# Kernel tuning notes

Hardware: AMD Instinct MI355X
Metric: run time of the kernel (lower is better)

## Reference

```python
import jax, jax.numpy as jnp
import numpy as np

N_HEADS = 16
D_EMBED = 1024
D_HEAD = D_EMBED // N_HEADS  # 64
B, S = 2, 2048


def setup_inputs() -> dict:
    key = jax.random.key(0)
    ks = jax.random.split(key, 6)
    k = jax.random.normal(ks[0], (B, S, D_EMBED), dtype=jnp.float32)
    q = jax.random.normal(ks[1], (B, S, D_EMBED), dtype=jnp.float32)
    v = jax.random.normal(ks[2], (B, S, D_EMBED), dtype=jnp.float32)
    # per-head projections, shared across heads (nn.Linear(d_head, d_head, bias=False))
    scale = 1.0 / np.sqrt(D_HEAD)
    Wk = jax.random.normal(ks[3], (D_HEAD, D_HEAD), dtype=jnp.float32) * scale
    Wq = jax.random.normal(ks[4], (D_HEAD, D_HEAD), dtype=jnp.float32) * scale
    Wv = jax.random.normal(ks[5], (D_HEAD, D_HEAD), dtype=jnp.float32) * scale
    return {"k": k, "q": q, "v": v, "Wk": Wk, "Wq": Wq, "Wv": Wv}


def reference(k, q, v, Wk, Wq, Wv):
    b, s, _ = k.shape
    # split heads: [b, s, h, dh]
    kh = k.reshape(b, s, N_HEADS, D_HEAD)
    qh = q.reshape(b, s, N_HEADS, D_HEAD)
    vh = v.reshape(b, s, N_HEADS, D_HEAD)
    # shared per-head linear projection (y = x @ W^T, torch Linear convention)
    kh = jnp.einsum('bshd,ed->bshe', kh, Wk)
    qh = jnp.einsum('bshd,ed->bshe', qh, Wq)
    vh = jnp.einsum('bshd,ed->bshe', vh, Wv)
    # attention scores [b, h, q, k]
    scores = jnp.einsum('bqhd,bkhd->bhqk', qh, kh) / np.sqrt(D_HEAD).astype(np.float32)
    attn = jax.nn.softmax(scores, axis=-1)
    out = jnp.einsum('bhqk,bkhd->bqhd', attn, vh)
    return out.reshape(b, s, D_EMBED)
```

## Files before the change

### kernel.cpp

```cpp
#include <hip/hip_runtime.h>
#include <hip/hip_bf16.h>

typedef unsigned short u16;
typedef __bf16 bf16x8 __attribute__((ext_vector_type(8)));
typedef float f32x4 __attribute__((ext_vector_type(4)));

#define S_LEN 2048
#define NH 16
#define NB 2
#define HEAD_ELEMS (NB * NH * S_LEN * 64)

#if __has_builtin(__builtin_amdgcn_exp2f)
#define EXP2(x) __builtin_amdgcn_exp2f(x)
#else
#define EXP2(x) exp2f(x)
#endif

#define QSCALE 0.180336880f
#define SHIFT2 30.0f

__device__ __forceinline__ bf16x8 pack8(float4 a, float4 b, float sc) {
    union { bf16x8 v; __hip_bfloat162 h[4]; } r;
    r.h[0] = __float22bfloat162_rn(make_float2(a.x * sc, a.y * sc));
    r.h[1] = __float22bfloat162_rn(make_float2(a.z * sc, a.w * sc));
    r.h[2] = __float22bfloat162_rn(make_float2(b.x * sc, b.y * sc));
    r.h[3] = __float22bfloat162_rn(make_float2(b.z * sc, b.w * sc));
    return r.v;
}

__global__ __launch_bounds__(256) void proj_kq(
    const float* __restrict__ kin, const float* __restrict__ qin,
    const float* __restrict__ Wk, const float* __restrict__ Wq,
    u16* __restrict__ Kh, u16* __restrict__ Qh)
{
    __shared__ __align__(16) u16 Yld[8 * 16 * 72];

    const int tid = threadIdx.x;
    const int wave = tid >> 6;
    const int lane = tid & 63;
    const int quad = lane >> 4;
    const int l15 = lane & 15;
    const int stile = blockIdx.x;
    const int p = blockIdx.y;
    const int hh = blockIdx.z;
    const long row0 = (long)stile * 16;
    const int b = (int)(row0 >> 11);
    const int s0 = (int)(row0 & 2047);

    const float* X = p ? qin : kin;
    const float* W = p ? Wq : Wk;
    const float sc = p ? QSCALE : 1.0f;

    const float* xr0 = X + (row0 + l15) * 1024 + (hh * 8 + wave * 2) * 64 + quad * 8;
    const float* xr1 = xr0 + 64;
    float4 xa[4], xb[4];
    xa[0] = *(const float4*)(xr0);      xa[1] = *(const float4*)(xr0 + 4);
    xa[2] = *(const float4*)(xr0 + 32); xa[3] = *(const float4*)(xr0 + 36);
    xb[0] = *(const float4*)(xr1);      xb[1] = *(const float4*)(xr1 + 4);
    xb[2] = *(const float4*)(xr1 + 32); xb[3] = *(const float4*)(xr1 + 36);

    bf16x8 wf[4][2];
    #pragma unroll
    for (int nt = 0; nt < 4; ++nt) {
        const float* wr = W + (nt * 16 + l15) * 64 + quad * 8;
        wf[nt][0] = pack8(*(const float4*)(wr),      *(const float4*)(wr + 4),  sc);
        wf[nt][1] = pack8(*(const float4*)(wr + 32), *(const float4*)(wr + 36), sc);
    }

    #pragma unroll
    for (int hp = 0; hp < 2; ++hp) {
        const int hl = wave * 2 + hp;
        bf16x8 a0 = pack8(hp ? xb[0] : xa[0], hp ? xb[1] : xa[1], 1.0f);
        bf16x8 a1 = pack8(hp ? xb[2] : xa[2], hp ? xb[3] : xa[3], 1.0f);
        #pragma unroll
        for (int nt = 0; nt < 4; ++nt) {
            f32x4 c = (f32x4){0.f, 0.f, 0.f, 0.f};
            c = __builtin_amdgcn_mfma_f32_16x16x32_bf16(a0, wf[nt][0], c, 0, 0, 0);
            c = __builtin_amdgcn_mfma_f32_16x16x32_bf16(a1, wf[nt][1], c, 0, 0, 0);
            union { __hip_bfloat162 h2; u16 u[2]; } x01, x23;
            x01.h2 = __float22bfloat162_rn(make_float2(c[0], c[1]));
            x23.h2 = __float22bfloat162_rn(make_float2(c[2], c[3]));
            int base = (hl * 16 + quad * 4) * 72 + nt * 16 + l15;
            Yld[base]       = x01.u[0];
            Yld[base + 72]  = x01.u[1];
            Yld[base + 144] = x23.u[0];
            Yld[base + 216] = x23.u[1];
        }
    }
    __syncthreads();

    u16* dst = p ? Qh : Kh;
    #pragma unroll
    for (int it = 0; it < 4; ++it) {
        int idx = tid + it * 256;
        int eg = idx & 7, s = (idx >> 3) & 15, hl = idx >> 7;
        int bh = b * NH + hh * 8 + hl;
        *(float4*)(dst + ((long)bh * S_LEN + s0 + s) * 64 + eg * 8) =
            *(const float4*)&Yld[(hl * 16 + s) * 72 + eg * 8];
    }
}

__global__ __launch_bounds__(256) void proj_v(
    const float* __restrict__ vin, const float* __restrict__ Wv, u16* __restrict__ Vt)
{
    __shared__ __align__(16) u16 Vtile[64 * 72];

    const int tid = threadIdx.x;
    const int wave = tid >> 6;
    const int lane = tid & 63;
    const int quad = lane >> 4;
    const int l15 = lane & 15;
    const long row0 = (long)blockIdx.x * 64;
    const int b = (int)(row0 >> 11);
    const int s0 = (int)(row0 & 2047);
    const int h = blockIdx.y;
    const int bh = b * NH + h;

    const float* xr = vin + (row0 + wave * 16 + l15) * 1024 + h * 64 + quad * 8;
    float4 x4[4];
    x4[0] = *(const float4*)(xr);      x4[1] = *(const float4*)(xr + 4);
    x4[2] = *(const float4*)(xr + 32); x4[3] = *(const float4*)(xr + 36);

    bf16x8 wf[4][2];
    #pragma unroll
    for (int dt = 0; dt < 4; ++dt) {
        const float* wr = Wv + (dt * 16 + l15) * 64 + quad * 8;
        wf[dt][0] = pack8(*(const float4*)(wr),      *(const float4*)(wr + 4),  1.0f);
        wf[dt][1] = pack8(*(const float4*)(wr + 32), *(const float4*)(wr + 36), 1.0f);
    }

    bf16x8 x0 = pack8(x4[0], x4[1], 1.0f);
    bf16x8 x1 = pack8(x4[2], x4[3], 1.0f);

    #pragma unroll
    for (int dt = 0; dt < 4; ++dt) {
        f32x4 c = (f32x4){0.f, 0.f, 0.f, 0.f};
        c = __builtin_amdgcn_mfma_f32_16x16x32_bf16(wf[dt][0], x0, c, 0, 0, 0);
        c = __builtin_amdgcn_mfma_f32_16x16x32_bf16(wf[dt][1], x1, c, 0, 0, 0);
        int base = (dt * 16 + quad * 4) * 72 + wave * 16 + l15;
        union { __hip_bfloat162 h2; u16 u[2]; } x01, x23;
        x01.h2 = __float22bfloat162_rn(make_float2(c[0], c[1]));
        x23.h2 = __float22bfloat162_rn(make_float2(c[2], c[3]));
        Vtile[base]       = x01.u[0];
        Vtile[base + 72]  = x01.u[1];
        Vtile[base + 144] = x23.u[0];
        Vtile[base + 216] = x23.u[1];
    }
    __syncthreads();

    u16* dst = Vt + (long)bh * 64 * S_LEN + s0;
    #pragma unroll
    for (int it = 0; it < 2; ++it) {
        int idx = tid + it * 256;
        int sg = idx & 7, e = idx >> 3;
        *(float4*)(dst + (long)e * S_LEN + sg * 8) = *(const float4*)&Vtile[e * 72 + sg * 8];
    }
}

__global__ __launch_bounds__(256, 2) void attn_kernel(
    const u16* __restrict__ Qh, const u16* __restrict__ Kh,
    const u16* __restrict__ Vt, float* __restrict__ out)
{
    __shared__ __align__(16) u16 Qld[64 * 72];
    __shared__ __align__(16) float Old[4][64 * 20];
    __shared__ float lbc[4][64];

    const int tid = threadIdx.x;
    const int wave = tid >> 6;
    const int lane = tid & 63;
    const int quad = lane >> 4;
    const int l15 = lane & 15;
    const int qb = blockIdx.x;
    const int bh = blockIdx.y;
    const int b = bh >> 4, h = bh & 15;
    const int q0 = qb * 64;
    const u16* kb = Kh + (long)bh * S_LEN * 64;
    const u16* vb = Vt + (long)bh * 64 * S_LEN;

    {
        const u16* qp = Qh + ((long)bh * S_LEN + q0) * 64;
        #pragma unroll
        for (int i = 0; i < 2; ++i) {
            int idx = tid + i * 256;
            int row = idx >> 3, gg = idx & 7;
            *(float4*)&Qld[row * 72 + gg * 8] = *(const float4*)(qp + row * 64 + gg * 8);
        }
    }
    __syncthreads();

    const int krow_off = ((l15 >> 2) * 8 + (l15 & 3)) * 64;

    f32x4 oacc[4][4];
    #pragma unroll
    for (int g = 0; g < 4; ++g)
        #pragma unroll
        for (int dt = 0; dt < 4; ++dt) oacc[g][dt] = (f32x4){0.f, 0.f, 0.f, 0.f};
    float rs[4] = {0.f, 0.f, 0.f, 0.f};

    for (int kt = wave; kt < S_LEN / 64; kt += 4) {
        const u16* kt_p = kb + (long)kt * 4096;
        const u16* vt_p = vb + kt * 64;
        #pragma unroll
        for (int c = 0; c < 2; ++c) {
            bf16x8 kf[2][2], vf[4];
            #pragma unroll
            for (int nn = 0; nn < 2; ++nn) {
                const u16* kr = kt_p + c * 2048 + krow_off + nn * 256 + quad * 8;
                kf[nn][0] = *(const bf16x8*)(kr);
                kf[nn][1] = *(const bf16x8*)(kr + 32);
            }
            #pragma unroll
            for (int dt = 0; dt < 4; ++dt)
                vf[dt] = *(const bf16x8*)(vt_p + (long)(dt * 16 + l15) * S_LEN + c * 32 + quad * 8);

            #pragma unroll
            for (int g = 0; g < 4; ++g) {
                const u16* qrow = &Qld[(g * 16 + l15) * 72 + quad * 8];
                bf16x8 qb0 = *(const bf16x8*)(qrow);
                bf16x8 qb1 = *(const bf16x8*)(qrow + 32);
                f32x4 s0 = (f32x4){0.f, 0.f, 0.f, 0.f};
                f32x4 s1 = (f32x4){0.f, 0.f, 0.f, 0.f};
                s0 = __builtin_amdgcn_mfma_f32_16x16x32_bf16(kf[0][0], qb0, s0, 0, 0, 0);
                s0 = __builtin_amdgcn_mfma_f32_16x16x32_bf16(kf[0][1], qb1, s0, 0, 0, 0);
                s1 = __builtin_amdgcn_mfma_f32_16x16x32_bf16(kf[1][0], qb0, s1, 0, 0, 0);
                s1 = __builtin_amdgcn_mfma_f32_16x16x32_bf16(kf[1][1], qb1, s1, 0, 0, 0);

                float p00 = EXP2(s0[0] - SHIFT2), p01 = EXP2(s0[1] - SHIFT2);
                float p02 = EXP2(s0[2] - SHIFT2), p03 = EXP2(s0[3] - SHIFT2);
                float p10 = EXP2(s1[0] - SHIFT2), p11 = EXP2(s1[1] - SHIFT2);
                float p12 = EXP2(s1[2] - SHIFT2), p13 = EXP2(s1[3] - SHIFT2);
                rs[g] += ((p00 + p01) + (p02 + p03)) + ((p10 + p11) + (p12 + p13));

                union { bf16x8 v; __hip_bfloat162 h2[4]; } pf;
                pf.h2[0] = __float22bfloat162_rn(make_float2(p00, p01));
                pf.h2[1] = __float22bfloat162_rn(make_float2(p02, p03));
                pf.h2[2] = __float22bfloat162_rn(make_float2(p10, p11));
                pf.h2[3] = __float22bfloat162_rn(make_float2(p12, p13));

                #pragma unroll
                for (int dt = 0; dt < 4; ++dt)
                    oacc[g][dt] = __builtin_amdgcn_mfma_f32_16x16x32_bf16(vf[dt], pf.v, oacc[g][dt], 0, 0, 0);
            }
        }
    }

    #pragma unroll
    for (int g = 0; g < 4; ++g) {
        rs[g] += __shfl_xor(rs[g], 16);
        rs[g] += __shfl_xor(rs[g], 32);
    }
    if (lane < 16) {
        #pragma unroll
        for (int g = 0; g < 4; ++g) lbc[wave][g * 16 + lane] = rs[g];
    }
    __syncthreads();

    const int rq = tid >> 2, seg = tid & 3;
    const float linv = 1.0f / (lbc[0][rq] + lbc[1][rq] + lbc[2][rq] + lbc[3][rq]);
    float* op = out + ((long)(b * S_LEN + q0 + rq)) * 1024 + h * 64;

    #pragma unroll
    for (int ph = 0; ph < 4; ++ph) {
        #pragma unroll
        for (int g = 0; g < 4; ++g)
            *(f32x4*)&Old[wave][(g * 16 + l15) * 20 + quad * 4] = oacc[g][ph];
        __syncthreads();
        f32x4 a = (f32x4){0.f, 0.f, 0.f, 0.f};
        #pragma unroll
        for (int w = 0; w < 4; ++w) a += *(const f32x4*)&Old[w][rq * 20 + seg * 4];
        *(float4*)(op + ph * 16 + seg * 4) =
            make_float4(a[0] * linv, a[1] * linv, a[2] * linv, a[3] * linv);
        __syncthreads();
    }
}

extern "C" void kernel_launch(void* const* d_in, const int* in_sizes, int n_in,
                              void* d_out, int out_size, void* d_ws, size_t ws_size,
                              hipStream_t stream) {
    const float* kin = (const float*)d_in[0];
    const float* qin = (const float*)d_in[1];
    const float* vin = (const float*)d_in[2];
    const float* Wk  = (const float*)d_in[3];
    const float* Wq  = (const float*)d_in[4];
    const float* Wv  = (const float*)d_in[5];
    float* out = (float*)d_out;

    u16* wsp = (u16*)d_ws;
    u16* Kh = wsp;
    u16* Qh = wsp + (long)HEAD_ELEMS;
    u16* Vt = wsp + 2 * (long)HEAD_ELEMS;

    dim3 kqg(256, 2, 2);
    proj_kq<<<kqg, 256, 0, stream>>>(kin, qin, Wk, Wq, Kh, Qh);
    dim3 vg(64, 16);
    proj_v<<<vg, 256, 0, stream>>>(vin, Wv, Vt);
    dim3 g(S_LEN / 64, NB * NH);
    attn_kernel<<<g, 256, 0, stream>>>(Qh, Kh, Vt, out);
}
```

Baseline: 177.2 us.

## Fuse projection kernels, halve attention query tile, remap blocks, fold shift into MFMA init

Merges the K/Q and V projection kernels into one launch that dispatches on block index, saving one kernel launch. The attention kernel now processes 32 query rows per block instead of 64, doubling the grid to 2048 blocks. Block indices are remapped so that neighbouring blocks spread across heads, which is meant to improve occupancy and load balance. The softmax shift constant is folded into the MFMA accumulator initialisation, removing a subtraction per score. Smaller query tiles mean each K/V tile is reloaded more times in total, and half the threads sit idle during the output epilogue.

```diff
diff --git a/kernel.cpp b/kernel.cpp
--- a/kernel.cpp
+++ b/kernel.cpp
@@ -28,10 +28,12 @@
     return r.v;
 }
 
-__global__ __launch_bounds__(256) void proj_kq(
+__global__ __launch_bounds__(256) void proj_fused(
     const float* __restrict__ kin, const float* __restrict__ qin,
+    const float* __restrict__ vin,
     const float* __restrict__ Wk, const float* __restrict__ Wq,
-    u16* __restrict__ Kh, u16* __restrict__ Qh)
+    const float* __restrict__ Wv,
+    u16* __restrict__ Kh, u16* __restrict__ Qh, u16* __restrict__ Vt)
 {
     __shared__ __align__(16) u16 Yld[8 * 16 * 72];
 
@@ -40,162 +42,154 @@
     const int lane = tid & 63;
     const int quad = lane >> 4;
     const int l15 = lane & 15;
-    const int stile = blockIdx.x;
-    const int p = blockIdx.y;
-    const int hh = blockIdx.z;
-    const long row0 = (long)stile * 16;
-    const int b = (int)(row0 >> 11);
-    const int s0 = (int)(row0 & 2047);
-
-    const float* X = p ? qin : kin;
-    const float* W = p ? Wq : Wk;
-    const float sc = p ? QSCALE : 1.0f;
-
-    const float* xr0 = X + (row0 + l15) * 1024 + (hh * 8 + wave * 2) * 64 + quad * 8;
-    const float* xr1 = xr0 + 64;
-    float4 xa[4], xb[4];
-    xa[0] = *(const float4*)(xr0);      xa[1] = *(const float4*)(xr0 + 4);
-    xa[2] = *(const float4*)(xr0 + 32); xa[3] = *(const float4*)(xr0 + 36);
-    xb[0] = *(const float4*)(xr1);      xb[1] = *(const float4*)(xr1 + 4);
-    xb[2] = *(const float4*)(xr1 + 32); xb[3] = *(const float4*)(xr1 + 36);
-
-    bf16x8 wf[4][2];
-    #pragma unroll
-    for (int nt = 0; nt < 4; ++nt) {
-        const float* wr = W + (nt * 16 + l15) * 64 + quad * 8;
-        wf[nt][0] = pack8(*(const float4*)(wr),      *(const float4*)(wr + 4),  sc);
-        wf[nt][1] = pack8(*(const float4*)(wr + 32), *(const float4*)(wr + 36), sc);
-    }
-
-    #pragma unroll
-    for (int hp = 0; hp < 2; ++hp) {
-        const int hl = wave * 2 + hp;
-        bf16x8 a0 = pack8(hp ? xb[0] : xa[0], hp ? xb[1] : xa[1], 1.0f);
-        bf16x8 a1 = pack8(hp ? xb[2] : xa[2], hp ? xb[3] : xa[3], 1.0f);
+    const int bid = blockIdx.x;
+
+    if (bid < 1024) {
+        const int stile = bid & 255;
+        const int p = (bid >> 8) & 1;
+        const int hh = bid >> 9;
+        const long row0 = (long)stile * 16;
+        const int b = (int)(row0 >> 11);
+        const int s0 = (int)(row0 & 2047);
+
+        const float* X = p ? qin : kin;
+        const float* W = p ? Wq : Wk;
+        const float sc = p ? QSCALE : 1.0f;
+
+        const float* xr0 = X + (row0 + l15) * 1024 + (hh * 8 + wave * 2) * 64 + quad * 8;
+        const float* xr1 = xr0 + 64;
+        float4 xa[4], xb[4];
+        xa[0] = *(const float4*)(xr0);      xa[1] = *(const float4*)(xr0 + 4);
+        xa[2] = *(const float4*)(xr0 + 32); xa[3] = *(const float4*)(xr0 + 36);
+        xb[0] = *(const float4*)(xr1);      xb[1] = *(const float4*)(xr1 + 4);
+        xb[2] = *(const float4*)(xr1 + 32); xb[3] = *(const float4*)(xr1 + 36);
+
+        bf16x8 wf[4][2];
         #pragma unroll
         for (int nt = 0; nt < 4; ++nt) {
+            const float* wr = W + (nt * 16 + l15) * 64 + quad * 8;
+            wf[nt][0] = pack8(*(const float4*)(wr),      *(const float4*)(wr + 4),  sc);
+            wf[nt][1] = pack8(*(const float4*)(wr + 32), *(const float4*)(wr + 36), sc);
+        }
+
+        #pragma unroll
+        for (int hp = 0; hp < 2; ++hp) {
+            const int hl = wave * 2 + hp;
+            bf16x8 a0 = pack8(hp ? xb[0] : xa[0], hp ? xb[1] : xa[1], 1.0f);
+            bf16x8 a1 = pack8(hp ? xb[2] : xa[2], hp ? xb[3] : xa[3], 1.0f);
+            #pragma unroll
+            for (int nt = 0; nt < 4; ++nt) {
+                f32x4 c = (f32x4){0.f, 0.f, 0.f, 0.f};
+                c = __builtin_amdgcn_mfma_f32_16x16x32_bf16(a0, wf[nt][0], c, 0, 0, 0);
+                c = __builtin_amdgcn_mfma_f32_16x16x32_bf16(a1, wf[nt][1], c, 0, 0, 0);
+                union { __hip_bfloat162 h2; u16 u[2]; } x01, x23;
+                x01.h2 = __float22bfloat162_rn(make_float2(c[0], c[1]));
+                x23.h2 = __float22bfloat162_rn(make_float2(c[2], c[3]));
+                int base = (hl * 16 + quad * 4) * 72 + nt * 16 + l15;
+                Yld[base]       = x01.u[0];
+                Yld[base + 72]  = x01.u[1];
+                Yld[base + 144] = x23.u[0];
+                Yld[base + 216] = x23.u[1];
+            }
+        }
+        __syncthreads();
+
+        u16* dst = p ? Qh : Kh;
+        #pragma unroll
+        for (int it = 0; it < 4; ++it) {
+            int idx = tid + it * 256;
+            int eg = idx & 7, s = (idx >> 3) & 15, hl = idx >> 7;
+            int bh = b * NH + hh * 8 + hl;
+            *(float4*)(dst + ((long)bh * S_LEN + s0 + s) * 64 + eg * 8) =
+                *(const float4*)&Yld[(hl * 16 + s) * 72 + eg * 8];
+        }
+    } else {
+        const int vid = bid - 1024;
+        const long row0 = (long)(vid & 63) * 64;
+        const int b = (int)(row0 >> 11);
+        const int s0 = (int)(row0 & 2047);
+        const int h = vid >> 6;
+        const int bh = b * NH + h;
+
+        const float* xr = vin + (row0 + wave * 16 + l15) * 1024 + h * 64 + quad * 8;
+        float4 x4[4];
+        x4[0] = *(const float4*)(xr);      x4[1] = *(const float4*)(xr + 4);
+        x4[2] = *(const float4*)(xr + 32); x4[3] = *(const float4*)(xr + 36);
+
+        bf16x8 wf[4][2];
+        #pragma unroll
+        for (int dt = 0; dt < 4; ++dt) {
+            const float* wr = Wv + (dt * 16 + l15) * 64 + quad * 8;
+            wf[dt][0] = pack8(*(const float4*)(wr),      *(const float4*)(wr + 4),  1.0f);
+            wf[dt][1] = pack8(*(const float4*)(wr + 32), *(const float4*)(wr + 36), 1.0f);
+        }
+
+        bf16x8 x0 = pack8(x4[0], x4[1], 1.0f);
+        bf16x8 x1 = pack8(x4[2], x4[3], 1.0f);
+
+        #pragma unroll
+        for (int dt = 0; dt < 4; ++dt) {
             f32x4 c = (f32x4){0.f, 0.f, 0.f, 0.f};
-            c = __builtin_amdgcn_mfma_f32_16x16x32_bf16(a0, wf[nt][0], c, 0, 0, 0);
-            c = __builtin_amdgcn_mfma_f32_16x16x32_bf16(a1, wf[nt][1], c, 0, 0, 0);
+            c = __builtin_amdgcn_mfma_f32_16x16x32_bf16(wf[dt][0], x0, c, 0, 0, 0);
+            c = __builtin_amdgcn_mfma_f32_16x16x32_bf16(wf[dt][1], x1, c, 0, 0, 0);
+            int base = (dt * 16 + quad * 4) * 72 + wave * 16 + l15;
             union { __hip_bfloat162 h2; u16 u[2]; } x01, x23;
             x01.h2 = __float22bfloat162_rn(make_float2(c[0], c[1]));
             x23.h2 = __float22bfloat162_rn(make_float2(c[2], c[3]));
-            int base = (hl * 16 + quad * 4) * 72 + nt * 16 + l15;
             Yld[base]       = x01.u[0];
             Yld[base + 72]  = x01.u[1];
             Yld[base + 144] = x23.u[0];
             Yld[base + 216] = x23.u[1];
         }
-    }
-    __syncthreads();
-
-    u16* dst = p ? Qh : Kh;
-    #pragma unroll
-    for (int it = 0; it < 4; ++it) {
-        int idx = tid + it * 256;
-        int eg = idx & 7, s = (idx >> 3) & 15, hl = idx >> 7;
-        int bh = b * NH + hh * 8 + hl;
-        *(float4*)(dst + ((long)bh * S_LEN + s0 + s) * 64 + eg * 8) =
-            *(const float4*)&Yld[(hl * 16 + s) * 72 + eg * 8];
-    }
-}
-
-__global__ __launch_bounds__(256) void proj_v(
-    const float* __restrict__ vin, const float* __restrict__ Wv, u16* __restrict__ Vt)
+        __syncthreads();
+
+        u16* dst = Vt + (long)bh * 64 * S_LEN + s0;
+        #pragma unroll
+        for (int it = 0; it < 2; ++it) {
+            int idx = tid + it * 256;
+            int sg = idx & 7, e = idx >> 3;
+            *(float4*)(dst + (long)e * S_LEN + sg * 8) = *(const float4*)&Yld[e * 72 + sg * 8];
+        }
+    }
+}
+
+__global__ __launch_bounds__(256, 2) void attn_kernel(
+    const u16* __restrict__ Qh, const u16* __restrict__ Kh,
+    const u16* __restrict__ Vt, float* __restrict__ out)
 {
-    __shared__ __align__(16) u16 Vtile[64 * 72];
+    __shared__ __align__(16) u16 Qld[32 * 72];
+    __shared__ __align__(16) float Old[4][32 * 20];
+    __shared__ float lbc[4][32];
 
     const int tid = threadIdx.x;
     const int wave = tid >> 6;
     const int lane = tid & 63;
     const int quad = lane >> 4;
     const int l15 = lane & 15;
-    const long row0 = (long)blockIdx.x * 64;
-    const int b = (int)(row0 >> 11);
-    const int s0 = (int)(row0 & 2047);
-    const int h = blockIdx.y;
-    const int bh = b * NH + h;
-
-    const float* xr = vin + (row0 + wave * 16 + l15) * 1024 + h * 64 + quad * 8;
-    float4 x4[4];
-    x4[0] = *(const float4*)(xr);      x4[1] = *(const float4*)(xr + 4);
-    x4[2] = *(const float4*)(xr + 32); x4[3] = *(const float4*)(xr + 36);
-
-    bf16x8 wf[4][2];
-    #pragma unroll
-    for (int dt = 0; dt < 4; ++dt) {
-        const float* wr = Wv + (dt * 16 + l15) * 64 + quad * 8;
-        wf[dt][0] = pack8(*(const float4*)(wr),      *(const float4*)(wr + 4),  1.0f);
-        wf[dt][1] = pack8(*(const float4*)(wr + 32), *(const float4*)(wr + 36), 1.0f);
-    }
-
-    bf16x8 x0 = pack8(x4[0], x4[1], 1.0f);
-    bf16x8 x1 = pack8(x4[2], x4[3], 1.0f);
-
-    #pragma unroll
-    for (int dt = 0; dt < 4; ++dt) {
-        f32x4 c = (f32x4){0.f, 0.f, 0.f, 0.f};
-        c = __builtin_amdgcn_mfma_f32_16x16x32_bf16(wf[dt][0], x0, c, 0, 0, 0);
-        c = __builtin_amdgcn_mfma_f32_16x16x32_bf16(wf[dt][1], x1, c, 0, 0, 0);
-        int base = (dt * 16 + quad * 4) * 72 + wave * 16 + l15;
-        union { __hip_bfloat162 h2; u16 u[2]; } x01, x23;
-        x01.h2 = __float22bfloat162_rn(make_float2(c[0], c[1]));
-        x23.h2 = __float22bfloat162_rn(make_float2(c[2], c[3]));
-        Vtile[base]       = x01.u[0];
-        Vtile[base + 72]  = x01.u[1];
-        Vtile[base + 144] = x23.u[0];
-        Vtile[base + 216] = x23.u[1];
-    }
-    __syncthreads();
-
-    u16* dst = Vt + (long)bh * 64 * S_LEN + s0;
-    #pragma unroll
-    for (int it = 0; it < 2; ++it) {
-        int idx = tid + it * 256;
-        int sg = idx & 7, e = idx >> 3;
-        *(float4*)(dst + (long)e * S_LEN + sg * 8) = *(const float4*)&Vtile[e * 72 + sg * 8];
-    }
-}
-
-__global__ __launch_bounds__(256, 2) void attn_kernel(
-    const u16* __restrict__ Qh, const u16* __restrict__ Kh,
-    const u16* __restrict__ Vt, float* __restrict__ out)
-{
-    __shared__ __align__(16) u16 Qld[64 * 72];
-    __shared__ __align__(16) float Old[4][64 * 20];
-    __shared__ float lbc[4][64];
-
-    const int tid = threadIdx.x;
-    const int wave = tid >> 6;
-    const int lane = tid & 63;
-    const int quad = lane >> 4;
-    const int l15 = lane & 15;
-    const int qb = blockIdx.x;
-    const int bh = blockIdx.y;
+    const int bid = blockIdx.x;
+    const int i = bid >> 3;
+    const int bh = (bid & 7) * 4 + (i >> 6);
+    const int qb = i & 63;
     const int b = bh >> 4, h = bh & 15;
-    const int q0 = qb * 64;
+    const int q0 = qb * 32;
     const u16* kb = Kh + (long)bh * S_LEN * 64;
     const u16* vb = Vt + (long)bh * 64 * S_LEN;
 
     {
         const u16* qp = Qh + ((long)bh * S_LEN + q0) * 64;
-        #pragma unroll
-        for (int i = 0; i < 2; ++i) {
-            int idx = tid + i * 256;
-            int row = idx >> 3, gg = idx & 7;
-            *(float4*)&Qld[row * 72 + gg * 8] = *(const float4*)(qp + row * 64 + gg * 8);
-        }
+        int row = tid >> 3, gg = tid & 7;
+        *(float4*)&Qld[row * 72 + gg * 8] = *(const float4*)(qp + row * 64 + gg * 8);
     }
     __syncthreads();
 
     const int krow_off = ((l15 >> 2) * 8 + (l15 & 3)) * 64;
 
-    f32x4 oacc[4][4];
+    f32x4 oacc[2][4];
     #pragma unroll
-    for (int g = 0; g < 4; ++g)
+    for (int g = 0; g < 2; ++g)
         #pragma unroll
         for (int dt = 0; dt < 4; ++dt) oacc[g][dt] = (f32x4){0.f, 0.f, 0.f, 0.f};
-    float rs[4] = {0.f, 0.f, 0.f, 0.f};
+    float rs[2] = {0.f, 0.f};
 
     for (int kt = wave; kt < S_LEN / 64; kt += 4) {
         const u16* kt_p = kb + (long)kt * 4096;
@@ -214,21 +208,21 @@
                 vf[dt] = *(const bf16x8*)(vt_p + (long)(dt * 16 + l15) * S_LEN + c * 32 + quad * 8);
 
             #pragma unroll
-            for (int g = 0; g < 4; ++g) {
+            for (int g = 0; g < 2; ++g) {
                 const u16* qrow = &Qld[(g * 16 + l15) * 72 + quad * 8];
                 bf16x8 qb0 = *(const bf16x8*)(qrow);
                 bf16x8 qb1 = *(const bf16x8*)(qrow + 32);
-                f32x4 s0 = (f32x4){0.f, 0.f, 0.f, 0.f};
-                f32x4 s1 = (f32x4){0.f, 0.f, 0.f, 0.f};
+                f32x4 s0 = (f32x4){-SHIFT2, -SHIFT2, -SHIFT2, -SHIFT2};
+                f32x4 s1 = (f32x4){-SHIFT2, -SHIFT2, -SHIFT2, -SHIFT2};
                 s0 = __builtin_amdgcn_mfma_f32_16x16x32_bf16(kf[0][0], qb0, s0, 0, 0, 0);
                 s0 = __builtin_amdgcn_mfma_f32_16x16x32_bf16(kf[0][1], qb1, s0, 0, 0, 0);
                 s1 = __builtin_amdgcn_mfma_f32_16x16x32_bf16(kf[1][0], qb0, s1, 0, 0, 0);
                 s1 = __builtin_amdgcn_mfma_f32_16x16x32_bf16(kf[1][1], qb1, s1, 0, 0, 0);
 
-                float p00 = EXP2(s0[0] - SHIFT2), p01 = EXP2(s0[1] - SHIFT2);
-                float p02 = EXP2(s0[2] - SHIFT2), p03 = EXP2(s0[3] - SHIFT2);
-                float p10 = EXP2(s1[0] - SHIFT2), p11 = EXP2(s1[1] - SHIFT2);
-                float p12 = EXP2(s1[2] - SHIFT2), p13 = EXP2(s1[3] - SHIFT2);
+                float p00 = EXP2(s0[0]), p01 = EXP2(s0[1]);
+                float p02 = EXP2(s0[2]), p03 = EXP2(s0[3]);
+                float p10 = EXP2(s1[0]), p11 = EXP2(s1[1]);
+                float p12 = EXP2(s1[2]), p13 = EXP2(s1[3]);
                 rs[g] += ((p00 + p01) + (p02 + p03)) + ((p10 + p11) + (p12 + p13));
 
                 union { bf16x8 v; __hip_bfloat162 h2[4]; } pf;
@@ -245,31 +239,34 @@
     }
 
     #pragma unroll
-    for (int g = 0; g < 4; ++g) {
+    for (int g = 0; g < 2; ++g) {
         rs[g] += __shfl_xor(rs[g], 16);
         rs[g] += __shfl_xor(rs[g], 32);
     }
     if (lane < 16) {
         #pragma unroll
-        for (int g = 0; g < 4; ++g) lbc[wave][g * 16 + lane] = rs[g];
+        for (int g = 0; g < 2; ++g) lbc[wave][g * 16 + lane] = rs[g];
     }
     __syncthreads();
 
-    const int rq = tid >> 2, seg = tid & 3;
-    const float linv = 1.0f / (lbc[0][rq] + lbc[1][rq] + lbc[2][rq] + lbc[3][rq]);
+    const int rq = (tid & 127) >> 2, seg = tid & 3;
+    float linv = 0.f;
+    if (tid < 128) linv = 1.0f / (lbc[0][rq] + lbc[1][rq] + lbc[2][rq] + lbc[3][rq]);
     float* op = out + ((long)(b * S_LEN + q0 + rq)) * 1024 + h * 64;
 
     #pragma unroll
     for (int ph = 0; ph < 4; ++ph) {
         #pragma unroll
-        for (int g = 0; g < 4; ++g)
+        for (int g = 0; g < 2; ++g)
             *(f32x4*)&Old[wave][(g * 16 + l15) * 20 + quad * 4] = oacc[g][ph];
         __syncthreads();
-        f32x4 a = (f32x4){0.f, 0.f, 0.f, 0.f};
-        #pragma unroll
-        for (int w = 0; w < 4; ++w) a += *(const f32x4*)&Old[w][rq * 20 + seg * 4];
-        *(float4*)(op + ph * 16 + seg * 4) =
-            make_float4(a[0] * linv, a[1] * linv, a[2] * linv, a[3] * linv);
+        if (tid < 128) {
+            f32x4 a = (f32x4){0.f, 0.f, 0.f, 0.f};
+            #pragma unroll
+            for (int w = 0; w < 4; ++w) a += *(const f32x4*)&Old[w][rq * 20 + seg * 4];
+            *(float4*)(op + ph * 16 + seg * 4) =
+                make_float4(a[0] * linv, a[1] * linv, a[2] * linv, a[3] * linv);
+        }
         __syncthreads();
     }
 }
@@ -290,10 +287,6 @@
     u16* Qh = wsp + (long)HEAD_ELEMS;
     u16* Vt = wsp + 2 * (long)HEAD_ELEMS;
 
-    dim3 kqg(256, 2, 2);
-    proj_kq<<<kqg, 256, 0, stream>>>(kin, qin, Wk, Wq, Kh, Qh);
-    dim3 vg(64, 16);
-    proj_v<<<vg, 256, 0, stream>>>(vin, Wv, Vt);
-    dim3 g(S_LEN / 64, NB * NH);
-    attn_kernel<<<g, 256, 0, stream>>>(Qh, Kh, Vt, out);
-}
+    proj_fused<<<dim3(2048), 256, 0, stream>>>(kin, qin, vin, Wk, Wq, Wv, Kh, Qh, Vt);
+    attn_kernel<<<dim3(2048), 256, 0, stream>>>(Qh, Kh, Vt, out);
+}
```

After: 228.3 us. 28.8% more time.
